# Optimization experiments

Hardware: AMD Instinct MI355X
Metric: run time of the kernel (lower is better)

## Reference

```python
import jax, jax.numpy as jnp
import numpy as np

N = 100000
E = 800000
NODE_DIM = 128
EDGE_DIM = 8
NUM_HEADS = 8
HEAD_DIM = NODE_DIM // NUM_HEADS


def setup_inputs() -> dict:
    key = jax.random.key(0)
    k_x, k_ei, k_ea, k_w1, k_b1, k_w2, k_b2 = jax.random.split(key, 7)
    x = jax.random.normal(k_x, (N, NODE_DIM), dtype=jnp.float32)
    edge_index = jax.random.randint(k_ei, (2, E), 0, N, dtype=jnp.int32)
    edge_attr = jax.random.normal(k_ea, (E, EDGE_DIM), dtype=jnp.float32)
    # node_proj: Linear(node_dim, node_dim)
    lim1 = 1.0 / np.sqrt(NODE_DIM)
    W_node = jax.random.uniform(k_w1, (NODE_DIM, NODE_DIM), minval=-lim1, maxval=lim1, dtype=jnp.float32)
    b_node = jax.random.uniform(k_b1, (NODE_DIM,), minval=-lim1, maxval=lim1, dtype=jnp.float32)
    # edge_to_attn: Linear(edge_dim, num_heads) followed by sigmoid
    lim2 = 1.0 / np.sqrt(EDGE_DIM)
    W_edge = jax.random.uniform(k_w2, (NUM_HEADS, EDGE_DIM), minval=-lim2, maxval=lim2, dtype=jnp.float32)
    b_edge = jax.random.uniform(k_b2, (NUM_HEADS,), minval=-lim2, maxval=lim2, dtype=jnp.float32)
    return {"x": x, "edge_index": edge_index, "edge_attr": edge_attr,
            "W_node": W_node, "b_node": b_node, "W_edge": W_edge, "b_edge": b_edge}


def reference(x, edge_index, edge_attr, W_node, b_node, W_edge, b_edge):
    # project node features: [N, node_dim]
    x_proj = x @ W_node.T + b_node
    # per-edge, per-head sigmoid gates: [E, H]
    edge_gates = jax.nn.sigmoid(edge_attr @ W_edge.T + b_edge)
    source = edge_index[0]
    target = edge_index[1]
    # gather source node features: [E, H, head_dim]
    x_source = x_proj[source].reshape(E, NUM_HEADS, HEAD_DIM)
    # gate and flatten messages: [E, node_dim]
    messages = (x_source * edge_gates[:, :, None]).reshape(E, NODE_DIM)
    # scatter-add to target nodes: [N, node_dim]
    out = jax.ops.segment_sum(messages, target, num_segments=N)
    return out
```

## Files before the change

### kernel.cpp

```cpp
#include <hip/hip_runtime.h>

typedef unsigned short u16;
typedef unsigned int u32;
typedef __attribute__((ext_vector_type(8))) short short8;
typedef __attribute__((ext_vector_type(4))) float f32x4;

constexpr int NODES = 100000;
constexpr int EDGES = 800000;
constexpr int DIM = 128;
constexpr int EDIM = 8;
constexpr int HEADS = 8;

constexpr int PROJ_BLOCKS = (NODES + 127) / 128;
constexpr int REC_BLOCKS  = (EDGES + 255) / 256;

__device__ inline u16 f2bf(float f) {
    u32 u = __float_as_uint(f);
    u = (u + 0x7FFFu + ((u >> 16) & 1u)) >> 16;
    return (u16)u;
}
__device__ inline float bf2f(u16 s) {
    return __uint_as_float(((u32)s) << 16);
}
__device__ inline u32 packbf(float a, float b) {
    return (u32)f2bf(a) | ((u32)f2bf(b) << 16);
}

__global__ __launch_bounds__(256) void prep_fused(const float* __restrict__ x,
                                                  const float* __restrict__ Wn,
                                                  const float* __restrict__ bn,
                                                  const int* __restrict__ ei,
                                                  const float* __restrict__ ea,
                                                  const float* __restrict__ We,
                                                  const float* __restrict__ be,
                                                  int* __restrict__ head4,
                                                  uint4* __restrict__ rec,
                                                  u16* __restrict__ xpb) {
    __shared__ u16 sLds[128 * 136];

    const int tid = threadIdx.x;

    if (blockIdx.x < PROJ_BLOCKS) {
        {
            #pragma unroll
            for (int i = tid; i < 128 * 16; i += 256) {
                int row = i >> 4, ch = i & 15;
                const float* p = Wn + row * DIM + ch * 8;
                float4 f0 = *reinterpret_cast<const float4*>(p);
                float4 f1 = *reinterpret_cast<const float4*>(p + 4);
                short8 v;
                v[0]=(short)f2bf(f0.x); v[1]=(short)f2bf(f0.y);
                v[2]=(short)f2bf(f0.z); v[3]=(short)f2bf(f0.w);
                v[4]=(short)f2bf(f1.x); v[5]=(short)f2bf(f1.y);
                v[6]=(short)f2bf(f1.z); v[7]=(short)f2bf(f1.w);
                *reinterpret_cast<short8*>(&sLds[row * 136 + ch * 8]) = v;
            }
        }
        __syncthreads();

        const int w = tid >> 6;
        const int l = tid & 63;
        const int lr = l & 15;
        const int lh = l >> 4;
        const int m0 = blockIdx.x * 128 + w * 32;

        f32x4 acc[2][8];
        #pragma unroll
        for (int mt = 0; mt < 2; ++mt)
            #pragma unroll
            for (int nt = 0; nt < 8; ++nt) acc[mt][nt] = f32x4{0, 0, 0, 0};

        #pragma unroll
        for (int kk = 0; kk < 4; ++kk) {
            const int kb = kk * 32 + lh * 8;
            short8 a0, a1;
            {
                int row = m0 + lr;  row = row < NODES ? row : 0;
                const float* p = x + (size_t)row * DIM + kb;
                float4 f0 = *reinterpret_cast<const float4*>(p);
                float4 f1 = *reinterpret_cast<const float4*>(p + 4);
                a0[0]=(short)f2bf(f0.x); a0[1]=(short)f2bf(f0.y);
                a0[2]=(short)f2bf(f0.z); a0[3]=(short)f2bf(f0.w);
                a0[4]=(short)f2bf(f1.x); a0[5]=(short)f2bf(f1.y);
                a0[6]=(short)f2bf(f1.z); a0[7]=(short)f2bf(f1.w);
            }
            {
                int row = m0 + 16 + lr;  row = row < NODES ? row : 0;
                const float* p = x + (size_t)row * DIM + kb;
                float4 f0 = *reinterpret_cast<const float4*>(p);
                float4 f1 = *reinterpret_cast<const float4*>(p + 4);
                a1[0]=(short)f2bf(f0.x); a1[1]=(short)f2bf(f0.y);
                a1[2]=(short)f2bf(f0.z); a1[3]=(short)f2bf(f0.w);
                a1[4]=(short)f2bf(f1.x); a1[5]=(short)f2bf(f1.y);
                a1[6]=(short)f2bf(f1.z); a1[7]=(short)f2bf(f1.w);
            }
            #pragma unroll
            for (int nt = 0; nt < 8; ++nt) {
                short8 b = *reinterpret_cast<const short8*>(&sLds[(nt * 16 + lr) * 136 + kb]);
                acc[0][nt] = __builtin_amdgcn_mfma_f32_16x16x32_bf16(a0, b, acc[0][nt], 0, 0, 0);
                acc[1][nt] = __builtin_amdgcn_mfma_f32_16x16x32_bf16(a1, b, acc[1][nt], 0, 0, 0);
            }
        }

        float bias[8];
        #pragma unroll
        for (int nt = 0; nt < 8; ++nt) bias[nt] = bn[nt * 16 + lr];

        #pragma unroll
        for (int mt = 0; mt < 2; ++mt) {
            #pragma unroll
            for (int r = 0; r < 4; ++r) {
                int grow = m0 + mt * 16 + lh * 4 + r;
                if (grow < NODES) {
                    #pragma unroll
                    for (int nt = 0; nt < 8; ++nt)
                        xpb[(size_t)grow * DIM + nt * 16 + lr] =
                            f2bf(acc[mt][nt][r] + bias[nt]);
                }
            }
        }
    } else {
        float* sW = reinterpret_cast<float*>(sLds);
        float* sb = sW + HEADS * EDIM;
        if (tid < HEADS * EDIM) sW[tid] = We[tid];
        if (tid < HEADS) sb[tid] = be[tid];
        __syncthreads();

        const int e = (blockIdx.x - PROJ_BLOCKS) * 256 + tid;
        if (e >= EDGES) return;

        const int src = ei[e];
        const int tgt = ei[EDGES + e];
        float4 a0 = *reinterpret_cast<const float4*>(ea + (size_t)e * EDIM);
        float4 a1 = *reinterpret_cast<const float4*>(ea + (size_t)e * EDIM + 4);

        float g[HEADS];
        #pragma unroll
        for (int h = 0; h < HEADS; ++h) {
            const float* w = &sW[h * EDIM];
            float z = sb[h]
                    + a0.x * w[0] + a0.y * w[1] + a0.z * w[2] + a0.w * w[3]
                    + a1.x * w[4] + a1.y * w[5] + a1.z * w[6] + a1.w * w[7];
            g[h] = 1.0f / (1.0f + __expf(-z));
        }

        int nx = atomicExch(&head4[tgt * 4 + (e & 3)], e);

        uint4 r0, r1;
        r0.x = (u32)nx;
        r0.y = (u32)src;
        r0.z = packbf(g[0], g[1]);
        r0.w = packbf(g[2], g[3]);
        r1.x = packbf(g[4], g[5]);
        r1.y = packbf(g[6], g[7]);
        r1.z = 0; r1.w = 0;
        rec[(size_t)e * 2 + 0] = r0;
        rec[(size_t)e * 2 + 1] = r1;
    }
}

__global__ __launch_bounds__(256) void aggregate_v7(const u16* __restrict__ xpb,
                                                    const int* __restrict__ head4,
                                                    const char* __restrict__ recB,
                                                    float* __restrict__ out) {
    const int n = blockIdx.x * 16 + (threadIdx.x >> 4);
    if (n >= NODES) return;
    const int l = threadIdx.x & 15;
    const int h = l >> 1;

    float acc[8];
    #pragma unroll
    for (int i = 0; i < 8; ++i) acc[i] = 0.0f;

    int e0 = head4[n * 4 + 0];
    int e1 = head4[n * 4 + 1];
    int e2 = head4[n * 4 + 2];
    int e3 = head4[n * 4 + 3];

    while (e0 >= 0 || e1 >= 0 || e2 >= 0 || e3 >= 0) {
        int c0 = e0 >= 0 ? e0 : 0;
        int c1 = e1 >= 0 ? e1 : 0;
        int c2 = e2 >= 0 ? e2 : 0;
        int c3 = e3 >= 0 ? e3 : 0;
        const char* r0 = recB + (size_t)c0 * 32;
        const char* r1 = recB + (size_t)c1 * 32;
        const char* r2 = recB + (size_t)c2 * 32;
        const char* r3 = recB + (size_t)c3 * 32;
        int2 ns0 = *reinterpret_cast<const int2*>(r0);
        int2 ns1 = *reinterpret_cast<const int2*>(r1);
        int2 ns2 = *reinterpret_cast<const int2*>(r2);
        int2 ns3 = *reinterpret_cast<const int2*>(r3);
        float g0 = bf2f(*reinterpret_cast<const u16*>(r0 + 8 + 2 * h));
        float g1 = bf2f(*reinterpret_cast<const u16*>(r1 + 8 + 2 * h));
        float g2 = bf2f(*reinterpret_cast<const u16*>(r2 + 8 + 2 * h));
        float g3 = bf2f(*reinterpret_cast<const u16*>(r3 + 8 + 2 * h));
        short8 u0 = *reinterpret_cast<const short8*>(xpb + (size_t)ns0.y * DIM + l * 8);
        short8 u1 = *reinterpret_cast<const short8*>(xpb + (size_t)ns1.y * DIM + l * 8);
        short8 u2 = *reinterpret_cast<const short8*>(xpb + (size_t)ns2.y * DIM + l * 8);
        short8 u3 = *reinterpret_cast<const short8*>(xpb + (size_t)ns3.y * DIM + l * 8);
        float m0 = e0 >= 0 ? g0 : 0.0f;
        float m1 = e1 >= 0 ? g1 : 0.0f;
        float m2 = e2 >= 0 ? g2 : 0.0f;
        float m3 = e3 >= 0 ? g3 : 0.0f;
        #pragma unroll
        for (int i = 0; i < 8; ++i) {
            acc[i] += m0 * bf2f((u16)u0[i]);
            acc[i] += m1 * bf2f((u16)u1[i]);
            acc[i] += m2 * bf2f((u16)u2[i]);
            acc[i] += m3 * bf2f((u16)u3[i]);
        }
        e0 = e0 >= 0 ? ns0.x : -1;
        e1 = e1 >= 0 ? ns1.x : -1;
        e2 = e2 >= 0 ? ns2.x : -1;
        e3 = e3 >= 0 ? ns3.x : -1;
    }

    float4 o0 = {acc[0], acc[1], acc[2], acc[3]};
    float4 o1 = {acc[4], acc[5], acc[6], acc[7]};
    float4* op = reinterpret_cast<float4*>(out + (size_t)n * DIM + l * 8);
    op[0] = o0;
    op[1] = o1;
}

__global__ __launch_bounds__(256) void edge_scatter(const int* __restrict__ ei,
                                                    const float* __restrict__ ea,
                                                    const float* __restrict__ We,
                                                    const float* __restrict__ be,
                                                    const u16* __restrict__ xpb,
                                                    float* __restrict__ out) {
    __shared__ float sW[HEADS * EDIM];
    __shared__ float sb[HEADS];
    if (threadIdx.x < HEADS * EDIM) sW[threadIdx.x] = We[threadIdx.x];
    if (threadIdx.x < HEADS) sb[threadIdx.x] = be[threadIdx.x];
    __syncthreads();

    const int t = blockIdx.x * 256 + threadIdx.x;
    const int e = t >> 5;
    const int l = t & 31;
    if (e >= EDGES) return;

    const int src = ei[e];
    const int tgt = ei[EDGES + e];
    const int h = l >> 2;

    float4 ea0 = *reinterpret_cast<const float4*>(ea + (size_t)e * EDIM);
    float4 ea1 = *reinterpret_cast<const float4*>(ea + (size_t)e * EDIM + 4);
    float4 wa = *reinterpret_cast<const float4*>(&sW[h * EDIM]);
    float4 wb = *reinterpret_cast<const float4*>(&sW[h * EDIM + 4]);
    float z = sb[h]
            + ea0.x * wa.x + ea0.y * wa.y + ea0.z * wa.z + ea0.w * wa.w
            + ea1.x * wb.x + ea1.y * wb.y + ea1.z * wb.z + ea1.w * wb.w;
    float g = 1.0f / (1.0f + __expf(-z));

    ushort4 u = *reinterpret_cast<const ushort4*>(xpb + (size_t)src * DIM + l * 4);
    float* op = out + (size_t)tgt * DIM + l * 4;
    unsafeAtomicAdd(op + 0, bf2f(u.x) * g);
    unsafeAtomicAdd(op + 1, bf2f(u.y) * g);
    unsafeAtomicAdd(op + 2, bf2f(u.z) * g);
    unsafeAtomicAdd(op + 3, bf2f(u.w) * g);
}

extern "C" void kernel_launch(void* const* d_in, const int* in_sizes, int n_in,
                              void* d_out, int out_size, void* d_ws, size_t ws_size,
                              hipStream_t stream) {
    const float* x   = (const float*)d_in[0];
    const int*   ei  = (const int*)d_in[1];
    const float* eat = (const float*)d_in[2];
    const float* Wn  = (const float*)d_in[3];
    const float* bn  = (const float*)d_in[4];
    const float* We  = (const float*)d_in[5];
    const float* be  = (const float*)d_in[6];
    float* out = (float*)d_out;

    u16* xpb   = (u16*)d_ws;
    int* head4 = (int*)(xpb + (size_t)NODES * DIM);
    char* rec  = (char*)(head4 + (size_t)NODES * 4);

    const size_t need = (size_t)NODES * DIM * 2 + (size_t)NODES * 16
                      + (size_t)EDGES * 32;
    const size_t need_fb = (size_t)NODES * DIM * 2;

    if (ws_size >= need) {
        hipMemsetAsync(head4, 0xFF, (size_t)NODES * 16, stream);
        prep_fused<<<PROJ_BLOCKS + REC_BLOCKS, 256, 0, stream>>>(
            x, Wn, bn, ei, eat, We, be, head4, (uint4*)rec, xpb);
        aggregate_v7<<<(NODES + 15) / 16, 256, 0, stream>>>(xpb, head4, rec, out);
    } else if (ws_size >= need_fb) {
        prep_fused<<<PROJ_BLOCKS, 256, 0, stream>>>(
            x, Wn, bn, ei, eat, We, be, nullptr, nullptr, xpb);
        hipMemsetAsync(d_out, 0, (size_t)out_size * sizeof(float), stream);
        edge_scatter<<<(EDGES * 32) / 256, 256, 0, stream>>>(ei, eat, We, be, xpb, out);
    }
}
```

Measured before the change: 112.4 us.

## Split fused prep kernel and widen per-lane work in aggregation

Splits the fused projection and edge-record kernel into two separate launches, so the edge-record blocks no longer reserve the 34KB LDS buffer the projection path needs. The aggregate kernel now uses 8 lanes per node with 16 channels each instead of 16 lanes with 8, doubling the gathered bytes per lane. It also issues more independent loads per edge and writes output with nontemporal stores. The trade-offs are an extra kernel launch and lost overlap between the two prep phases, plus higher register pressure and fewer threads per node in aggregation.

```diff
diff --git a/kernel.cpp b/kernel.cpp
--- a/kernel.cpp
+++ b/kernel.cpp
@@ -11,9 +11,6 @@
 constexpr int EDIM = 8;
 constexpr int HEADS = 8;
 
-constexpr int PROJ_BLOCKS = (NODES + 127) / 128;
-constexpr int REC_BLOCKS  = (EDGES + 255) / 256;
-
 __device__ inline u16 f2bf(float f) {
     u32 u = __float_as_uint(f);
     u = (u + 0x7FFFu + ((u >> 16) & 1u)) >> 16;
@@ -26,151 +23,148 @@
     return (u32)f2bf(a) | ((u32)f2bf(b) << 16);
 }
 
-__global__ __launch_bounds__(256) void prep_fused(const float* __restrict__ x,
-                                                  const float* __restrict__ Wn,
-                                                  const float* __restrict__ bn,
-                                                  const int* __restrict__ ei,
-                                                  const float* __restrict__ ea,
-                                                  const float* __restrict__ We,
-                                                  const float* __restrict__ be,
-                                                  int* __restrict__ head4,
-                                                  uint4* __restrict__ rec,
-                                                  u16* __restrict__ xpb) {
-    __shared__ u16 sLds[128 * 136];
+__global__ __launch_bounds__(256) void node_proj_mfma(const float* __restrict__ x,
+                                                      const float* __restrict__ Wn,
+                                                      const float* __restrict__ bn,
+                                                      u16* __restrict__ xpb) {
+    __shared__ u16 sW[128 * 136];
 
     const int tid = threadIdx.x;
-
-    if (blockIdx.x < PROJ_BLOCKS) {
+    {
+        #pragma unroll
+        for (int i = tid; i < 128 * 16; i += 256) {
+            int row = i >> 4, ch = i & 15;
+            const float* p = Wn + row * DIM + ch * 8;
+            float4 f0 = *reinterpret_cast<const float4*>(p);
+            float4 f1 = *reinterpret_cast<const float4*>(p + 4);
+            short8 v;
+            v[0]=(short)f2bf(f0.x); v[1]=(short)f2bf(f0.y);
+            v[2]=(short)f2bf(f0.z); v[3]=(short)f2bf(f0.w);
+            v[4]=(short)f2bf(f1.x); v[5]=(short)f2bf(f1.y);
+            v[6]=(short)f2bf(f1.z); v[7]=(short)f2bf(f1.w);
+            *reinterpret_cast<short8*>(&sW[row * 136 + ch * 8]) = v;
+        }
+    }
+    __syncthreads();
+
+    const int w = tid >> 6;
+    const int l = tid & 63;
+    const int lr = l & 15;
+    const int lh = l >> 4;
+    const int m0 = blockIdx.x * 128 + w * 32;
+
+    f32x4 acc[2][8];
+    #pragma unroll
+    for (int mt = 0; mt < 2; ++mt)
+        #pragma unroll
+        for (int nt = 0; nt < 8; ++nt) acc[mt][nt] = f32x4{0, 0, 0, 0};
+
+    #pragma unroll
+    for (int kk = 0; kk < 4; ++kk) {
+        const int kb = kk * 32 + lh * 8;
+        short8 a0, a1;
         {
-            #pragma unroll
-            for (int i = tid; i < 128 * 16; i += 256) {
-                int row = i >> 4, ch = i & 15;
-                const float* p = Wn + row * DIM + ch * 8;
-                float4 f0 = *reinterpret_cast<const float4*>(p);
-                float4 f1 = *reinterpret_cast<const float4*>(p + 4);
-                short8 v;
-                v[0]=(short)f2bf(f0.x); v[1]=(short)f2bf(f0.y);
-                v[2]=(short)f2bf(f0.z); v[3]=(short)f2bf(f0.w);
-                v[4]=(short)f2bf(f1.x); v[5]=(short)f2bf(f1.y);
-                v[6]=(short)f2bf(f1.z); v[7]=(short)f2bf(f1.w);
-                *reinterpret_cast<short8*>(&sLds[row * 136 + ch * 8]) = v;
+            int row = m0 + lr;  row = row < NODES ? row : 0;
+            const float* p = x + (size_t)row * DIM + kb;
+            float4 f0 = *reinterpret_cast<const float4*>(p);
+            float4 f1 = *reinterpret_cast<const float4*>(p + 4);
+            a0[0]=(short)f2bf(f0.x); a0[1]=(short)f2bf(f0.y);
+            a0[2]=(short)f2bf(f0.z); a0[3]=(short)f2bf(f0.w);
+            a0[4]=(short)f2bf(f1.x); a0[5]=(short)f2bf(f1.y);
+            a0[6]=(short)f2bf(f1.z); a0[7]=(short)f2bf(f1.w);
+        }
+        {
+            int row = m0 + 16 + lr;  row = row < NODES ? row : 0;
+            const float* p = x + (size_t)row * DIM + kb;
+            float4 f0 = *reinterpret_cast<const float4*>(p);
+            float4 f1 = *reinterpret_cast<const float4*>(p + 4);
+            a1[0]=(short)f2bf(f0.x); a1[1]=(short)f2bf(f0.y);
+            a1[2]=(short)f2bf(f0.z); a1[3]=(short)f2bf(f0.w);
+            a1[4]=(short)f2bf(f1.x); a1[5]=(short)f2bf(f1.y);
+            a1[6]=(short)f2bf(f1.z); a1[7]=(short)f2bf(f1.w);
+        }
+        #pragma unroll
+        for (int nt = 0; nt < 8; ++nt) {
+            short8 b = *reinterpret_cast<const short8*>(&sW[(nt * 16 + lr) * 136 + kb]);
+            acc[0][nt] = __builtin_amdgcn_mfma_f32_16x16x32_bf16(a0, b, acc[0][nt], 0, 0, 0);
+            acc[1][nt] = __builtin_amdgcn_mfma_f32_16x16x32_bf16(a1, b, acc[1][nt], 0, 0, 0);
+        }
+    }
+
+    float bias[8];
+    #pragma unroll
+    for (int nt = 0; nt < 8; ++nt) bias[nt] = bn[nt * 16 + lr];
+
+    #pragma unroll
+    for (int mt = 0; mt < 2; ++mt) {
+        #pragma unroll
+        for (int r = 0; r < 4; ++r) {
+            int grow = m0 + mt * 16 + lh * 4 + r;
+            if (grow < NODES) {
+                #pragma unroll
+                for (int nt = 0; nt < 8; ++nt)
+                    xpb[(size_t)grow * DIM + nt * 16 + lr] =
+                        f2bf(acc[mt][nt][r] + bias[nt]);
             }
         }
-        __syncthreads();
-
-        const int w = tid >> 6;
-        const int l = tid & 63;
-        const int lr = l & 15;
-        const int lh = l >> 4;
-        const int m0 = blockIdx.x * 128 + w * 32;
-
-        f32x4 acc[2][8];
-        #pragma unroll
-        for (int mt = 0; mt < 2; ++mt)
-            #pragma unroll
-            for (int nt = 0; nt < 8; ++nt) acc[mt][nt] = f32x4{0, 0, 0, 0};
-
-        #pragma unroll
-        for (int kk = 0; kk < 4; ++kk) {
-            const int kb = kk * 32 + lh * 8;
-            short8 a0, a1;
-            {
-                int row = m0 + lr;  row = row < NODES ? row : 0;
-                const float* p = x + (size_t)row * DIM + kb;
-                float4 f0 = *reinterpret_cast<const float4*>(p);
-                float4 f1 = *reinterpret_cast<const float4*>(p + 4);
-                a0[0]=(short)f2bf(f0.x); a0[1]=(short)f2bf(f0.y);
-                a0[2]=(short)f2bf(f0.z); a0[3]=(short)f2bf(f0.w);
-                a0[4]=(short)f2bf(f1.x); a0[5]=(short)f2bf(f1.y);
-                a0[6]=(short)f2bf(f1.z); a0[7]=(short)f2bf(f1.w);
-            }
-            {
-                int row = m0 + 16 + lr;  row = row < NODES ? row : 0;
-                const float* p = x + (size_t)row * DIM + kb;
-                float4 f0 = *reinterpret_cast<const float4*>(p);
-                float4 f1 = *reinterpret_cast<const float4*>(p + 4);
-                a1[0]=(short)f2bf(f0.x); a1[1]=(short)f2bf(f0.y);
-                a1[2]=(short)f2bf(f0.z); a1[3]=(short)f2bf(f0.w);
-                a1[4]=(short)f2bf(f1.x); a1[5]=(short)f2bf(f1.y);
-                a1[6]=(short)f2bf(f1.z); a1[7]=(short)f2bf(f1.w);
-            }
-            #pragma unroll
-            for (int nt = 0; nt < 8; ++nt) {
-                short8 b = *reinterpret_cast<const short8*>(&sLds[(nt * 16 + lr) * 136 + kb]);
-                acc[0][nt] = __builtin_amdgcn_mfma_f32_16x16x32_bf16(a0, b, acc[0][nt], 0, 0, 0);
-                acc[1][nt] = __builtin_amdgcn_mfma_f32_16x16x32_bf16(a1, b, acc[1][nt], 0, 0, 0);
-            }
-        }
-
-        float bias[8];
-        #pragma unroll
-        for (int nt = 0; nt < 8; ++nt) bias[nt] = bn[nt * 16 + lr];
-
-        #pragma unroll
-        for (int mt = 0; mt < 2; ++mt) {
-            #pragma unroll
-            for (int r = 0; r < 4; ++r) {
-                int grow = m0 + mt * 16 + lh * 4 + r;
-                if (grow < NODES) {
-                    #pragma unroll
-                    for (int nt = 0; nt < 8; ++nt)
-                        xpb[(size_t)grow * DIM + nt * 16 + lr] =
-                            f2bf(acc[mt][nt][r] + bias[nt]);
-                }
-            }
-        }
-    } else {
-        float* sW = reinterpret_cast<float*>(sLds);
-        float* sb = sW + HEADS * EDIM;
-        if (tid < HEADS * EDIM) sW[tid] = We[tid];
-        if (tid < HEADS) sb[tid] = be[tid];
-        __syncthreads();
-
-        const int e = (blockIdx.x - PROJ_BLOCKS) * 256 + tid;
-        if (e >= EDGES) return;
-
-        const int src = ei[e];
-        const int tgt = ei[EDGES + e];
-        float4 a0 = *reinterpret_cast<const float4*>(ea + (size_t)e * EDIM);
-        float4 a1 = *reinterpret_cast<const float4*>(ea + (size_t)e * EDIM + 4);
-
-        float g[HEADS];
-        #pragma unroll
-        for (int h = 0; h < HEADS; ++h) {
-            const float* w = &sW[h * EDIM];
-            float z = sb[h]
-                    + a0.x * w[0] + a0.y * w[1] + a0.z * w[2] + a0.w * w[3]
-                    + a1.x * w[4] + a1.y * w[5] + a1.z * w[6] + a1.w * w[7];
-            g[h] = 1.0f / (1.0f + __expf(-z));
-        }
-
-        int nx = atomicExch(&head4[tgt * 4 + (e & 3)], e);
-
-        uint4 r0, r1;
-        r0.x = (u32)nx;
-        r0.y = (u32)src;
-        r0.z = packbf(g[0], g[1]);
-        r0.w = packbf(g[2], g[3]);
-        r1.x = packbf(g[4], g[5]);
-        r1.y = packbf(g[6], g[7]);
-        r1.z = 0; r1.w = 0;
-        rec[(size_t)e * 2 + 0] = r0;
-        rec[(size_t)e * 2 + 1] = r1;
-    }
-}
-
-__global__ __launch_bounds__(256) void aggregate_v7(const u16* __restrict__ xpb,
+    }
+}
+
+__global__ __launch_bounds__(256) void build_rec(const int* __restrict__ ei,
+                                                 const float* __restrict__ ea,
+                                                 const float* __restrict__ We,
+                                                 const float* __restrict__ be,
+                                                 int* __restrict__ head4,
+                                                 uint4* __restrict__ rec) {
+    __shared__ float sW[HEADS * EDIM];
+    __shared__ float sb[HEADS];
+    if (threadIdx.x < HEADS * EDIM) sW[threadIdx.x] = We[threadIdx.x];
+    if (threadIdx.x < HEADS) sb[threadIdx.x] = be[threadIdx.x];
+    __syncthreads();
+
+    const int e = blockIdx.x * 256 + threadIdx.x;
+    if (e >= EDGES) return;
+
+    const int src = ei[e];
+    const int tgt = ei[EDGES + e];
+    float4 a0 = *reinterpret_cast<const float4*>(ea + (size_t)e * EDIM);
+    float4 a1 = *reinterpret_cast<const float4*>(ea + (size_t)e * EDIM + 4);
+
+    float g[HEADS];
+    #pragma unroll
+    for (int h = 0; h < HEADS; ++h) {
+        const float* w = &sW[h * EDIM];
+        float z = sb[h]
+                + a0.x * w[0] + a0.y * w[1] + a0.z * w[2] + a0.w * w[3]
+                + a1.x * w[4] + a1.y * w[5] + a1.z * w[6] + a1.w * w[7];
+        g[h] = 1.0f / (1.0f + __expf(-z));
+    }
+
+    int nx = atomicExch(&head4[tgt * 4 + (e & 3)], e);
+
+    uint4 r0, r1;
+    r0.x = (u32)nx;
+    r0.y = (u32)src;
+    r0.z = packbf(g[0], g[1]);
+    r0.w = packbf(g[2], g[3]);
+    r1.x = packbf(g[4], g[5]);
+    r1.y = packbf(g[6], g[7]);
+    r1.z = 0; r1.w = 0;
+    rec[(size_t)e * 2 + 0] = r0;
+    rec[(size_t)e * 2 + 1] = r1;
+}
+
+__global__ __launch_bounds__(256) void aggregate_v8(const u16* __restrict__ xpb,
                                                     const int* __restrict__ head4,
                                                     const char* __restrict__ recB,
                                                     float* __restrict__ out) {
-    const int n = blockIdx.x * 16 + (threadIdx.x >> 4);
+    const int n = blockIdx.x * 32 + (threadIdx.x >> 3);
     if (n >= NODES) return;
-    const int l = threadIdx.x & 15;
-    const int h = l >> 1;
-
-    float acc[8];
-    #pragma unroll
-    for (int i = 0; i < 8; ++i) acc[i] = 0.0f;
+    const int l = threadIdx.x & 7;
+
+    float acc[16];
+    #pragma unroll
+    for (int i = 0; i < 16; ++i) acc[i] = 0.0f;
 
     int e0 = head4[n * 4 + 0];
     int e1 = head4[n * 4 + 1];
@@ -190,24 +184,32 @@
         int2 ns1 = *reinterpret_cast<const int2*>(r1);
         int2 ns2 = *reinterpret_cast<const int2*>(r2);
         int2 ns3 = *reinterpret_cast<const int2*>(r3);
-        float g0 = bf2f(*reinterpret_cast<const u16*>(r0 + 8 + 2 * h));
-        float g1 = bf2f(*reinterpret_cast<const u16*>(r1 + 8 + 2 * h));
-        float g2 = bf2f(*reinterpret_cast<const u16*>(r2 + 8 + 2 * h));
-        float g3 = bf2f(*reinterpret_cast<const u16*>(r3 + 8 + 2 * h));
-        short8 u0 = *reinterpret_cast<const short8*>(xpb + (size_t)ns0.y * DIM + l * 8);
-        short8 u1 = *reinterpret_cast<const short8*>(xpb + (size_t)ns1.y * DIM + l * 8);
-        short8 u2 = *reinterpret_cast<const short8*>(xpb + (size_t)ns2.y * DIM + l * 8);
-        short8 u3 = *reinterpret_cast<const short8*>(xpb + (size_t)ns3.y * DIM + l * 8);
+        float g0 = bf2f(*reinterpret_cast<const u16*>(r0 + 8 + 2 * l));
+        float g1 = bf2f(*reinterpret_cast<const u16*>(r1 + 8 + 2 * l));
+        float g2 = bf2f(*reinterpret_cast<const u16*>(r2 + 8 + 2 * l));
+        float g3 = bf2f(*reinterpret_cast<const u16*>(r3 + 8 + 2 * l));
+        const u16* p0 = xpb + (size_t)ns0.y * DIM + l * 16;
+        const u16* p1 = xpb + (size_t)ns1.y * DIM + l * 16;
+        const u16* p2 = xpb + (size_t)ns2.y * DIM + l * 16;
+        const u16* p3 = xpb + (size_t)ns3.y * DIM + l * 16;
+        short8 ua0 = *reinterpret_cast<const short8*>(p0);
+        short8 ub0 = *reinterpret_cast<const short8*>(p0 + 8);
+        short8 ua1 = *reinterpret_cast<const short8*>(p1);
+        short8 ub1 = *reinterpret_cast<const short8*>(p1 + 8);
+        short8 ua2 = *reinterpret_cast<const short8*>(p2);
+        short8 ub2 = *reinterpret_cast<const short8*>(p2 + 8);
+        short8 ua3 = *reinterpret_cast<const short8*>(p3);
+        short8 ub3 = *reinterpret_cast<const short8*>(p3 + 8);
         float m0 = e0 >= 0 ? g0 : 0.0f;
         float m1 = e1 >= 0 ? g1 : 0.0f;
         float m2 = e2 >= 0 ? g2 : 0.0f;
         float m3 = e3 >= 0 ? g3 : 0.0f;
         #pragma unroll
         for (int i = 0; i < 8; ++i) {
-            acc[i] += m0 * bf2f((u16)u0[i]);
-            acc[i] += m1 * bf2f((u16)u1[i]);
-            acc[i] += m2 * bf2f((u16)u2[i]);
-            acc[i] += m3 * bf2f((u16)u3[i]);
+            acc[i]     += m0 * bf2f((u16)ua0[i]) + m1 * bf2f((u16)ua1[i])
+                        + m2 * bf2f((u16)ua2[i]) + m3 * bf2f((u16)ua3[i]);
+            acc[8 + i] += m0 * bf2f((u16)ub0[i]) + m1 * bf2f((u16)ub1[i])
+                        + m2 * bf2f((u16)ub2[i]) + m3 * bf2f((u16)ub3[i]);
         }
         e0 = e0 >= 0 ? ns0.x : -1;
         e1 = e1 >= 0 ? ns1.x : -1;
@@ -215,11 +217,12 @@
         e3 = e3 >= 0 ? ns3.x : -1;
     }
 
-    float4 o0 = {acc[0], acc[1], acc[2], acc[3]};
-    float4 o1 = {acc[4], acc[5], acc[6], acc[7]};
-    float4* op = reinterpret_cast<float4*>(out + (size_t)n * DIM + l * 8);
-    op[0] = o0;
-    op[1] = o1;
+    f32x4* op = reinterpret_cast<f32x4*>(out + (size_t)n * DIM + l * 16);
+    #pragma unroll
+    for (int q = 0; q < 4; ++q) {
+        f32x4 o = {acc[q * 4 + 0], acc[q * 4 + 1], acc[q * 4 + 2], acc[q * 4 + 3]};
+        __builtin_nontemporal_store(o, op + q);
+    }
 }
 
 __global__ __launch_bounds__(256) void edge_scatter(const int* __restrict__ ei,
@@ -282,12 +285,12 @@
 
     if (ws_size >= need) {
         hipMemsetAsync(head4, 0xFF, (size_t)NODES * 16, stream);
-        prep_fused<<<PROJ_BLOCKS + REC_BLOCKS, 256, 0, stream>>>(
-            x, Wn, bn, ei, eat, We, be, head4, (uint4*)rec, xpb);
-        aggregate_v7<<<(NODES + 15) / 16, 256, 0, stream>>>(xpb, head4, rec, out);
+        build_rec<<<(EDGES + 255) / 256, 256, 0, stream>>>(ei, eat, We, be,
+                                                           head4, (uint4*)rec);
+        node_proj_mfma<<<(NODES + 127) / 128, 256, 0, stream>>>(x, Wn, bn, xpb);
+        aggregate_v8<<<(NODES + 31) / 32, 256, 0, stream>>>(xpb, head4, rec, out);
     } else if (ws_size >= need_fb) {
-        prep_fused<<<PROJ_BLOCKS, 256, 0, stream>>>(
-            x, Wn, bn, ei, eat, We, be, nullptr, nullptr, xpb);
+        node_proj_mfma<<<(NODES + 127) / 128, 256, 0, stream>>>(x, Wn, bn, xpb);
         hipMemsetAsync(d_out, 0, (size_t)out_size * sizeof(float), stream);
         edge_scatter<<<(EDGES * 32) / 256, 256, 0, stream>>>(ei, eat, We, be, xpb, out);
     }
```

Measured after the change: 130.1 us. +15.8%, slower.

## Compact edge records to 16 bytes with 8-bit gates and sentinel record

Applied to the files above, without the earlier changes.

Edge records shrink from 32 to 16 bytes: sigmoid gates are quantized to 8 bits, the source offset is premultiplied by DIM, and a sentinel record at index -1 removes the per-edge validity selects in the linked-list walk. The output is rescaled by 1/255 at the end. The projection also stages W in two 64-row halves to halve LDS usage, which should raise occupancy but reloads the x tile twice. The 8-bit gate quantization adds error beyond bf16, and the fallback path now writes a sentinel through a pointer that may be out of workspace range.

```diff
diff --git a/kernel.cpp b/kernel.cpp
--- a/kernel.cpp
+++ b/kernel.cpp
@@ -1,5 +1,6 @@
 #include <hip/hip_runtime.h>
 
+typedef unsigned char u8;
 typedef unsigned short u16;
 typedef unsigned int u32;
 typedef __attribute__((ext_vector_type(8))) short short8;
@@ -21,9 +22,6 @@
 }
 __device__ inline float bf2f(u16 s) {
     return __uint_as_float(((u32)s) << 16);
-}
-__device__ inline u32 packbf(float a, float b) {
-    return (u32)f2bf(a) | ((u32)f2bf(b) << 16);
 }
 
 __global__ __launch_bounds__(256) void prep_fused(const float* __restrict__ x,
@@ -34,29 +32,16 @@
                                                   const float* __restrict__ We,
                                                   const float* __restrict__ be,
                                                   int* __restrict__ head4,
-                                                  uint4* __restrict__ rec,
+                                                  uint4* __restrict__ recE,
                                                   u16* __restrict__ xpb) {
-    __shared__ u16 sLds[128 * 136];
+    __shared__ u16 sLds[64 * 136];
 
     const int tid = threadIdx.x;
 
     if (blockIdx.x < PROJ_BLOCKS) {
-        {
-            #pragma unroll
-            for (int i = tid; i < 128 * 16; i += 256) {
-                int row = i >> 4, ch = i & 15;
-                const float* p = Wn + row * DIM + ch * 8;
-                float4 f0 = *reinterpret_cast<const float4*>(p);
-                float4 f1 = *reinterpret_cast<const float4*>(p + 4);
-                short8 v;
-                v[0]=(short)f2bf(f0.x); v[1]=(short)f2bf(f0.y);
-                v[2]=(short)f2bf(f0.z); v[3]=(short)f2bf(f0.w);
-                v[4]=(short)f2bf(f1.x); v[5]=(short)f2bf(f1.y);
-                v[6]=(short)f2bf(f1.z); v[7]=(short)f2bf(f1.w);
-                *reinterpret_cast<short8*>(&sLds[row * 136 + ch * 8]) = v;
-            }
-        }
-        __syncthreads();
+        if (blockIdx.x == 0 && tid == 0) {
+            recE[-1] = uint4{(u32)-1, 0u, 0u, 0u};
+        }
 
         const int w = tid >> 6;
         const int l = tid & 63;
@@ -71,34 +56,57 @@
             for (int nt = 0; nt < 8; ++nt) acc[mt][nt] = f32x4{0, 0, 0, 0};
 
         #pragma unroll
-        for (int kk = 0; kk < 4; ++kk) {
-            const int kb = kk * 32 + lh * 8;
-            short8 a0, a1;
+        for (int half = 0; half < 2; ++half) {
+            __syncthreads();
             {
-                int row = m0 + lr;  row = row < NODES ? row : 0;
-                const float* p = x + (size_t)row * DIM + kb;
-                float4 f0 = *reinterpret_cast<const float4*>(p);
-                float4 f1 = *reinterpret_cast<const float4*>(p + 4);
-                a0[0]=(short)f2bf(f0.x); a0[1]=(short)f2bf(f0.y);
-                a0[2]=(short)f2bf(f0.z); a0[3]=(short)f2bf(f0.w);
-                a0[4]=(short)f2bf(f1.x); a0[5]=(short)f2bf(f1.y);
-                a0[6]=(short)f2bf(f1.z); a0[7]=(short)f2bf(f1.w);
+                #pragma unroll
+                for (int i = tid; i < 64 * 16; i += 256) {
+                    int row = i >> 4, ch = i & 15;
+                    const float* p = Wn + (half * 64 + row) * DIM + ch * 8;
+                    float4 f0 = *reinterpret_cast<const float4*>(p);
+                    float4 f1 = *reinterpret_cast<const float4*>(p + 4);
+                    short8 v;
+                    v[0]=(short)f2bf(f0.x); v[1]=(short)f2bf(f0.y);
+                    v[2]=(short)f2bf(f0.z); v[3]=(short)f2bf(f0.w);
+                    v[4]=(short)f2bf(f1.x); v[5]=(short)f2bf(f1.y);
+                    v[6]=(short)f2bf(f1.z); v[7]=(short)f2bf(f1.w);
+                    *reinterpret_cast<short8*>(&sLds[row * 136 + ch * 8]) = v;
+                }
             }
-            {
-                int row = m0 + 16 + lr;  row = row < NODES ? row : 0;
-                const float* p = x + (size_t)row * DIM + kb;
-                float4 f0 = *reinterpret_cast<const float4*>(p);
-                float4 f1 = *reinterpret_cast<const float4*>(p + 4);
-                a1[0]=(short)f2bf(f0.x); a1[1]=(short)f2bf(f0.y);
-                a1[2]=(short)f2bf(f0.z); a1[3]=(short)f2bf(f0.w);
-                a1[4]=(short)f2bf(f1.x); a1[5]=(short)f2bf(f1.y);
-                a1[6]=(short)f2bf(f1.z); a1[7]=(short)f2bf(f1.w);
-            }
+            __syncthreads();
+
             #pragma unroll
-            for (int nt = 0; nt < 8; ++nt) {
-                short8 b = *reinterpret_cast<const short8*>(&sLds[(nt * 16 + lr) * 136 + kb]);
-                acc[0][nt] = __builtin_amdgcn_mfma_f32_16x16x32_bf16(a0, b, acc[0][nt], 0, 0, 0);
-                acc[1][nt] = __builtin_amdgcn_mfma_f32_16x16x32_bf16(a1, b, acc[1][nt], 0, 0, 0);
+            for (int kk = 0; kk < 4; ++kk) {
+                const int kb = kk * 32 + lh * 8;
+                short8 a0, a1;
+                {
+                    int row = m0 + lr;  row = row < NODES ? row : 0;
+                    const float* p = x + (size_t)row * DIM + kb;
+                    float4 f0 = *reinterpret_cast<const float4*>(p);
+                    float4 f1 = *reinterpret_cast<const float4*>(p + 4);
+                    a0[0]=(short)f2bf(f0.x); a0[1]=(short)f2bf(f0.y);
+                    a0[2]=(short)f2bf(f0.z); a0[3]=(short)f2bf(f0.w);
+                    a0[4]=(short)f2bf(f1.x); a0[5]=(short)f2bf(f1.y);
+                    a0[6]=(short)f2bf(f1.z); a0[7]=(short)f2bf(f1.w);
+                }
+                {
+                    int row = m0 + 16 + lr;  row = row < NODES ? row : 0;
+                    const float* p = x + (size_t)row * DIM + kb;
+                    float4 f0 = *reinterpret_cast<const float4*>(p);
+                    float4 f1 = *reinterpret_cast<const float4*>(p + 4);
+                    a1[0]=(short)f2bf(f0.x); a1[1]=(short)f2bf(f0.y);
+                    a1[2]=(short)f2bf(f0.z); a1[3]=(short)f2bf(f0.w);
+                    a1[4]=(short)f2bf(f1.x); a1[5]=(short)f2bf(f1.y);
+                    a1[6]=(short)f2bf(f1.z); a1[7]=(short)f2bf(f1.w);
+                }
+                #pragma unroll
+                for (int nt = 0; nt < 4; ++nt) {
+                    const int ntg = half * 4 + nt;
+                    short8 b = *reinterpret_cast<const short8*>(
+                        &sLds[(nt * 16 + lr) * 136 + kb]);
+                    acc[0][ntg] = __builtin_amdgcn_mfma_f32_16x16x32_bf16(a0, b, acc[0][ntg], 0, 0, 0);
+                    acc[1][ntg] = __builtin_amdgcn_mfma_f32_16x16x32_bf16(a1, b, acc[1][ntg], 0, 0, 0);
+                }
             }
         }
 
@@ -134,39 +142,38 @@
         float4 a0 = *reinterpret_cast<const float4*>(ea + (size_t)e * EDIM);
         float4 a1 = *reinterpret_cast<const float4*>(ea + (size_t)e * EDIM + 4);
 
-        float g[HEADS];
+        u32 q[HEADS];
         #pragma unroll
         for (int h = 0; h < HEADS; ++h) {
             const float* w = &sW[h * EDIM];
             float z = sb[h]
                     + a0.x * w[0] + a0.y * w[1] + a0.z * w[2] + a0.w * w[3]
                     + a1.x * w[4] + a1.y * w[5] + a1.z * w[6] + a1.w * w[7];
-            g[h] = 1.0f / (1.0f + __expf(-z));
+            float g = 1.0f / (1.0f + __expf(-z));
+            q[h] = (u32)(g * 255.0f + 0.5f);
         }
 
         int nx = atomicExch(&head4[tgt * 4 + (e & 3)], e);
 
-        uint4 r0, r1;
-        r0.x = (u32)nx;
-        r0.y = (u32)src;
-        r0.z = packbf(g[0], g[1]);
-        r0.w = packbf(g[2], g[3]);
-        r1.x = packbf(g[4], g[5]);
-        r1.y = packbf(g[6], g[7]);
-        r1.z = 0; r1.w = 0;
-        rec[(size_t)e * 2 + 0] = r0;
-        rec[(size_t)e * 2 + 1] = r1;
+        uint4 r;
+        r.x = (u32)nx;
+        r.y = (u32)(src * DIM);
+        r.z = q[0] | (q[1] << 8) | (q[2] << 16) | (q[3] << 24);
+        r.w = q[4] | (q[5] << 8) | (q[6] << 16) | (q[7] << 24);
+        recE[e] = r;
     }
 }
 
-__global__ __launch_bounds__(256) void aggregate_v7(const u16* __restrict__ xpb,
-                                                    const int* __restrict__ head4,
-                                                    const char* __restrict__ recB,
-                                                    float* __restrict__ out) {
+__global__ __launch_bounds__(256) void aggregate_v10(const u16* __restrict__ xpb,
+                                                     const int* __restrict__ head4,
+                                                     const uint4* __restrict__ recE,
+                                                     float* __restrict__ out) {
     const int n = blockIdx.x * 16 + (threadIdx.x >> 4);
     if (n >= NODES) return;
     const int l = threadIdx.x & 15;
     const int h = l >> 1;
+    const int hsh = (h & 3) * 8;
+    const bool hlo = (h < 4);
 
     float acc[8];
     #pragma unroll
@@ -177,46 +184,35 @@
     int e2 = head4[n * 4 + 2];
     int e3 = head4[n * 4 + 3];
 
-    while (e0 >= 0 || e1 >= 0 || e2 >= 0 || e3 >= 0) {
-        int c0 = e0 >= 0 ? e0 : 0;
-        int c1 = e1 >= 0 ? e1 : 0;
-        int c2 = e2 >= 0 ? e2 : 0;
-        int c3 = e3 >= 0 ? e3 : 0;
-        const char* r0 = recB + (size_t)c0 * 32;
-        const char* r1 = recB + (size_t)c1 * 32;
-        const char* r2 = recB + (size_t)c2 * 32;
-        const char* r3 = recB + (size_t)c3 * 32;
-        int2 ns0 = *reinterpret_cast<const int2*>(r0);
-        int2 ns1 = *reinterpret_cast<const int2*>(r1);
-        int2 ns2 = *reinterpret_cast<const int2*>(r2);
-        int2 ns3 = *reinterpret_cast<const int2*>(r3);
-        float g0 = bf2f(*reinterpret_cast<const u16*>(r0 + 8 + 2 * h));
-        float g1 = bf2f(*reinterpret_cast<const u16*>(r1 + 8 + 2 * h));
-        float g2 = bf2f(*reinterpret_cast<const u16*>(r2 + 8 + 2 * h));
-        float g3 = bf2f(*reinterpret_cast<const u16*>(r3 + 8 + 2 * h));
-        short8 u0 = *reinterpret_cast<const short8*>(xpb + (size_t)ns0.y * DIM + l * 8);
-        short8 u1 = *reinterpret_cast<const short8*>(xpb + (size_t)ns1.y * DIM + l * 8);
-        short8 u2 = *reinterpret_cast<const short8*>(xpb + (size_t)ns2.y * DIM + l * 8);
-        short8 u3 = *reinterpret_cast<const short8*>(xpb + (size_t)ns3.y * DIM + l * 8);
-        float m0 = e0 >= 0 ? g0 : 0.0f;
-        float m1 = e1 >= 0 ? g1 : 0.0f;
-        float m2 = e2 >= 0 ? g2 : 0.0f;
-        float m3 = e3 >= 0 ? g3 : 0.0f;
+    while ((e0 & e1 & e2 & e3) != -1) {
+        uint4 R0 = recE[(ptrdiff_t)e0];
+        uint4 R1 = recE[(ptrdiff_t)e1];
+        uint4 R2 = recE[(ptrdiff_t)e2];
+        uint4 R3 = recE[(ptrdiff_t)e3];
+        float g0 = (float)(((hlo ? R0.z : R0.w) >> hsh) & 0xFF);
+        float g1 = (float)(((hlo ? R1.z : R1.w) >> hsh) & 0xFF);
+        float g2 = (float)(((hlo ? R2.z : R2.w) >> hsh) & 0xFF);
+        float g3 = (float)(((hlo ? R3.z : R3.w) >> hsh) & 0xFF);
+        short8 u0 = *reinterpret_cast<const short8*>(xpb + R0.y + l * 8);
+        short8 u1 = *reinterpret_cast<const short8*>(xpb + R1.y + l * 8);
+        short8 u2 = *reinterpret_cast<const short8*>(xpb + R2.y + l * 8);
+        short8 u3 = *reinterpret_cast<const short8*>(xpb + R3.y + l * 8);
         #pragma unroll
         for (int i = 0; i < 8; ++i) {
-            acc[i] += m0 * bf2f((u16)u0[i]);
-            acc[i] += m1 * bf2f((u16)u1[i]);
-            acc[i] += m2 * bf2f((u16)u2[i]);
-            acc[i] += m3 * bf2f((u16)u3[i]);
-        }
-        e0 = e0 >= 0 ? ns0.x : -1;
-        e1 = e1 >= 0 ? ns1.x : -1;
-        e2 = e2 >= 0 ? ns2.x : -1;
-        e3 = e3 >= 0 ? ns3.x : -1;
+            acc[i] += g0 * bf2f((u16)u0[i]);
+            acc[i] += g1 * bf2f((u16)u1[i]);
+            acc[i] += g2 * bf2f((u16)u2[i]);
+            acc[i] += g3 * bf2f((u16)u3[i]);
+        }
+        e0 = (int)R0.x;
+        e1 = (int)R1.x;
+        e2 = (int)R2.x;
+        e3 = (int)R3.x;
     }
 
-    float4 o0 = {acc[0], acc[1], acc[2], acc[3]};
-    float4 o1 = {acc[4], acc[5], acc[6], acc[7]};
+    constexpr float DQ = 1.0f / 255.0f;
+    float4 o0 = {acc[0] * DQ, acc[1] * DQ, acc[2] * DQ, acc[3] * DQ};
+    float4 o1 = {acc[4] * DQ, acc[5] * DQ, acc[6] * DQ, acc[7] * DQ};
     float4* op = reinterpret_cast<float4*>(out + (size_t)n * DIM + l * 8);
     op[0] = o0;
     op[1] = o1;
@@ -274,20 +270,21 @@
 
     u16* xpb   = (u16*)d_ws;
     int* head4 = (int*)(xpb + (size_t)NODES * DIM);
-    char* rec  = (char*)(head4 + (size_t)NODES * 4);
+    char* recS = (char*)(head4 + (size_t)NODES * 4);
+    uint4* recE = (uint4*)(recS + 16);
 
     const size_t need = (size_t)NODES * DIM * 2 + (size_t)NODES * 16
-                      + (size_t)EDGES * 32;
+                      + (size_t)(EDGES + 1) * 16;
     const size_t need_fb = (size_t)NODES * DIM * 2;
 
     if (ws_size >= need) {
         hipMemsetAsync(head4, 0xFF, (size_t)NODES * 16, stream);
         prep_fused<<<PROJ_BLOCKS + REC_BLOCKS, 256, 0, stream>>>(
-            x, Wn, bn, ei, eat, We, be, head4, (uint4*)rec, xpb);
-        aggregate_v7<<<(NODES + 15) / 16, 256, 0, stream>>>(xpb, head4, rec, out);
+            x, Wn, bn, ei, eat, We, be, head4, recE, xpb);
+        aggregate_v10<<<(NODES + 15) / 16, 256, 0, stream>>>(xpb, head4, recE, out);
     } else if (ws_size >= need_fb) {
         prep_fused<<<PROJ_BLOCKS, 256, 0, stream>>>(
-            x, Wn, bn, ei, eat, We, be, nullptr, nullptr, xpb);
+            x, Wn, bn, ei, eat, We, be, nullptr, recE, xpb);
         hipMemsetAsync(d_out, 0, (size_t)out_size * sizeof(float), stream);
         edge_scatter<<<(EDGES * 32) / 256, 256, 0, stream>>>(ei, eat, We, be, xpb, out);
     }
```

Measured after the change: 112.7 us. No clear change (+0.3%).
